# Optimization experiments

Measured on AMD Instinct MI355X. Metric: run time of the kernel, lower is better.

Reference implementation:

```python
import jax, jax.numpy as jnp
import numpy as np

EMB = 256
N_NODES = 100000
N_EDGES = 500000
N_REL = 10
REL_DIM = 64
HID = 128
HEADS = 4
HEAD_DIM = HID // HEADS


def setup_inputs() -> dict:
    key = jax.random.key(0)
    ks = jax.random.split(key, 16)
    s = lambda i, shape: jax.random.normal(ks[i], shape, dtype=jnp.float32) * 0.05
    return {
        "node_embeddings": jax.random.normal(ks[0], (N_NODES, EMB), dtype=jnp.float32),
        "edge_index": jax.random.randint(ks[1], (2, N_EDGES), 0, N_NODES),
        "relation_type": jax.random.randint(ks[2], (N_EDGES,), 0, N_REL),
        "rel_emb": s(3, (N_REL, REL_DIM)),
        "W_edge": s(4, (2 * EMB, HID)), "b_edge": jnp.zeros((HID,), jnp.float32),
        "W_q": s(5, (REL_DIM, HID)), "b_q": jnp.zeros((HID,), jnp.float32),
        "W_k": s(6, (HID, HID)), "b_k": jnp.zeros((HID,), jnp.float32),
        "W_v": s(7, (HID, HID)), "b_v": jnp.zeros((HID,), jnp.float32),
        "W_o1": s(8, (HID, HID)), "b_o1": jnp.zeros((HID,), jnp.float32),
        "W_o2": s(9, (HID, 1)), "b_o2": jnp.zeros((1,), jnp.float32),
    }


def reference(node_embeddings, edge_index, relation_type, rel_emb,
              W_edge, b_edge, W_q, b_q, W_k, b_k, W_v, b_v,
              W_o1, b_o1, W_o2, b_o2):
    # Gather endpoint features: [E, 2*EMB]
    src = node_embeddings[edge_index[0]]
    tgt = node_embeddings[edge_index[1]]
    edge_features = jnp.concatenate([src, tgt], axis=1)
    # Edge MLP (dropout is identity at eval): [E, HID]
    edge_hidden = jax.nn.relu(edge_features @ W_edge + b_edge)
    # Relation embedding lookup: [E, REL_DIM]
    rel = rel_emb[relation_type]
    E = edge_hidden.shape[0]
    Q = (rel @ W_q + b_q).reshape(E, HEADS, HEAD_DIM)
    K = (edge_hidden @ W_k + b_k).reshape(E, HEADS, HEAD_DIM)
    V = (edge_hidden @ W_v + b_v).reshape(E, HEADS, HEAD_DIM)
    scale = jnp.sqrt(jnp.float32(HEAD_DIM))
    scores = jnp.sum(Q * K, axis=-1) / scale          # [E, HEADS]
    attn = jax.nn.softmax(scores, axis=-1)            # softmax over heads
    attended = (attn[..., None] * V).reshape(E, HID)
    output = attended + edge_hidden
    # Output MLP: Linear->ReLU->Linear(1)
    h = jax.nn.relu(output @ W_o1 + b_o1)
    score = (h @ W_o2 + b_o2).squeeze(-1)             # [E]
    return score
```

## Files before the change

### kernel.cpp

```cpp
#include <hip/hip_runtime.h>

#define EMB   256
#define HID   128
#define RELD  64
#define NREL  10
#define TE    64

typedef __attribute__((ext_vector_type(8)))  short bf16x8;
typedef __attribute__((ext_vector_type(16))) float f32x16;

__device__ __forceinline__ float bf16_to_f32(unsigned short u) {
    union { unsigned int i; float f; } v;
    v.i = ((unsigned int)u) << 16;
    return v.f;
}

__device__ __forceinline__ unsigned short f32_to_bf16(float x) {
    union { unsigned int i; float f; } v;
    v.f = x;
    unsigned int b = v.i;
    unsigned int rounded = b + 0x7fffu + ((b >> 16) & 1u);
    return (unsigned short)(rounded >> 16);
}

template <bool F32>
__device__ __forceinline__ float ldx(const void* p, size_t i) {
    if (F32) return ((const float*)p)[i];
    return bf16_to_f32(((const unsigned short*)p)[i]);
}

__device__ __forceinline__ bool detect_f32(const void* nodeEmb) {
    const float* f = (const float*)nodeEmb;
    float x = f[(threadIdx.x & 63) * 997];
    bool sane = isfinite(x) && fabsf(x) < 1.0e6f;
    unsigned long long m = __ballot(sane);
    return __popcll(m) >= 48;
}

template <bool F32>
__device__ void prep_body(int vb, const void* W_edge, const void* W_k,
                          const void* W_v, const void* W_o1, const void* rel_emb,
                          const void* W_q, const void* b_q,
                          unsigned short* WTe, unsigned short* WTk,
                          unsigned short* WTv, unsigned short* WTo1, float* Qtab)
{
    if (vb < 448) {
        int idx = vb * 256 + threadIdx.x;
        if (idx < 65536) {
            int kc = idx >> 12, e = idx & 4095;
            int g = e >> 3, j = e & 7;
            int col = g & 127, kg = g >> 7;
            int k = kc * 32 + kg * 8 + j;
            WTe[idx] = f32_to_bf16(ldx<F32>(W_edge, (size_t)k * HID + col));
        } else if (idx < 65536 + 16384) {
            int i = idx - 65536;
            int kc = i >> 12, e = i & 4095;
            int g = e >> 3, j = e & 7;
            int col = g & 127, kg = (g >> 7) & 3;
            int k = kc * 32 + kg * 8 + j;
            WTk[i] = f32_to_bf16(ldx<F32>(W_k, (size_t)k * HID + col));
        } else if (idx < 65536 + 2 * 16384) {
            int i = idx - 65536 - 16384;
            int kc = i >> 12, e = i & 4095;
            int g = e >> 3, j = e & 7;
            int col = g & 127, kg = (g >> 7) & 3;
            int k = kc * 32 + kg * 8 + j;
            WTv[i] = f32_to_bf16(ldx<F32>(W_v, (size_t)k * HID + col));
        } else {
            int i = idx - 65536 - 2 * 16384;
            int kc = i >> 12, e = i & 4095;
            int g = e >> 3, j = e & 7;
            int col = g & 127, kg = (g >> 7) & 3;
            int k = kc * 32 + kg * 8 + j;
            WTo1[i] = f32_to_bf16(ldx<F32>(W_o1, (size_t)k * HID + col));
        }
    } else {
        const int t = threadIdx.x;
        const int c = t & (HID - 1);
        const int h = t >> 7;
        for (int r = h; r < NREL; r += 2) {
            float acc = 0.f;
            for (int d = 0; d < RELD; ++d)
                acc += ldx<F32>(rel_emb, r * RELD + d) * ldx<F32>(W_q, (size_t)d * HID + c);
            Qtab[r * HID + c] = acc + ldx<F32>(b_q, c);
        }
    }
}

__global__ void prep_kernel(const void* nodeEmb,
                            const void* W_edge, const void* W_k, const void* W_v,
                            const void* W_o1, const void* rel_emb, const void* W_q,
                            const void* b_q,
                            unsigned short* WTe, unsigned short* WTk,
                            unsigned short* WTv, unsigned short* WTo1, float* Qtab,
                            unsigned short* nodeBf16, int convBlocks,
                            unsigned long long nodeElems)
{
    bool f32 = detect_f32(nodeEmb);
    int b = blockIdx.x;
    if (b < convBlocks) {
        if (!f32) return;
        unsigned long long i = (unsigned long long)b * 2048ull + threadIdx.x * 8;
        if (i + 8 <= nodeElems) {
            const float* src = (const float*)nodeEmb + i;
            float4 f0 = *(const float4*)src;
            float4 f1 = *(const float4*)(src + 4);
            union { unsigned short us[8]; uint4 v; } pk;
            pk.us[0] = f32_to_bf16(f0.x); pk.us[1] = f32_to_bf16(f0.y);
            pk.us[2] = f32_to_bf16(f0.z); pk.us[3] = f32_to_bf16(f0.w);
            pk.us[4] = f32_to_bf16(f1.x); pk.us[5] = f32_to_bf16(f1.y);
            pk.us[6] = f32_to_bf16(f1.z); pk.us[7] = f32_to_bf16(f1.w);
            *(uint4*)(nodeBf16 + i) = pk.v;
        }
        return;
    }
    b -= convBlocks;
    if (f32) prep_body<true >(b, W_edge, W_k, W_v, W_o1, rel_emb, W_q, b_q,
                              WTe, WTk, WTv, WTo1, Qtab);
    else     prep_body<false>(b, W_edge, W_k, W_v, W_o1, rel_emb, W_q, b_q,
                              WTe, WTk, WTv, WTo1, Qtab);
}

struct __align__(16) Smem {
    unsigned short sHid[TE][136];
    union {
        unsigned short sA[TE][40];
        float sQf[NREL * HID];
    } u;
    unsigned short sB[4096];
    float sBias[5 * HID];
    float sSc[TE][4], sAttn[TE][4];
    float sPart[TE][2];
    int   sSrc[TE], sTgt[TE], sRel[TE];
};

__device__ __forceinline__ void gemm128(Smem& sm, const unsigned short* WT,
                                        f32x16* acc, int t, int rt, int cg2,
                                        int c, int h5)
{
    for (int kc = 0; kc < 4; ++kc) {
        const unsigned short* base = WT + kc * 4096;
        __syncthreads();
        *(uint4*)&sm.sB[(size_t)t * 8]         = *(const uint4*)(base + (size_t)t * 8);
        *(uint4*)&sm.sB[(size_t)(t + 256) * 8] = *(const uint4*)(base + (size_t)(t + 256) * 8);
        __syncthreads();
        #pragma unroll
        for (int s = 0; s < 2; ++s) {
            bf16x8 a = *(const bf16x8*)&sm.sHid[32 * rt + c][kc * 32 + s * 16 + h5 * 8];
            #pragma unroll
            for (int ct = 0; ct < 2; ++ct) {
                bf16x8 b = *(const bf16x8*)
                    &sm.sB[((s * 2 + h5) * 128 + 64 * cg2 + 32 * ct + c) * 8];
                acc[ct] = __builtin_amdgcn_mfma_f32_32x32x16_bf16(a, b, acc[ct], 0, 0, 0);
            }
        }
    }
}

template <bool F32, bool GBF16>
__device__ void fused_body(
    Smem& sm,
    const void* gsrc, const int* edgeIdx, const int* relType,
    const unsigned short* WTe, const unsigned short* WTk,
    const unsigned short* WTv, const unsigned short* WTo1,
    const void* b_edge, const void* b_k, const void* b_v,
    const void* b_o1, const void* W_o2, const void* b_o2,
    const float* Qtab, void* outp, int E)
{
    const int t   = threadIdx.x;
    const int l   = t & 63;
    const int w   = t >> 6;
    const int c   = l & 31;
    const int h5  = l >> 5;
    const int rt  = w & 1;
    const int cg2 = w >> 1;
    const int bs  = blockIdx.x * TE;

    if (t < TE) {
        int e = bs + t;
        if (e >= E) e = E - 1;
        if (e < 0)  e = 0;
        sm.sSrc[t] = edgeIdx[e];
        sm.sTgt[t] = edgeIdx[E + e];
        int r = relType[e];
        if (r < 0) r = 0;
        if (r >= NREL) r = NREL - 1;
        sm.sRel[t] = r;
    }
    for (int i = t; i < 5 * HID; i += 256) {
        int which = i >> 7, j = i & (HID - 1);
        float v = (which == 0) ? ldx<F32>(b_edge, j)
                : (which == 1) ? ldx<F32>(b_k, j)
                : (which == 2) ? ldx<F32>(b_v, j)
                : (which == 3) ? ldx<F32>(b_o1, j)
                               : ldx<F32>(W_o2, j);
        sm.sBias[i] = v;
    }
    __syncthreads();

    const int edge_s = t >> 2;
    const int grp    = t & 3;

    f32x16 acc[2];
    acc[0] = (f32x16)(0.0f); acc[1] = (f32x16)(0.0f);
    for (int kc = 0; kc < 16; ++kc) {
        __syncthreads();
        {
            int node = (kc < 8) ? sm.sSrc[edge_s] : sm.sTgt[edge_s];
            int col0 = (kc & 7) * 32 + grp * 8;
            if (GBF16) {
                *(uint4*)&sm.u.sA[edge_s][grp * 8] =
                    *(const uint4*)((const unsigned short*)gsrc +
                                    (size_t)node * EMB + col0);
            } else {
                const float* p = (const float*)gsrc + (size_t)node * EMB + col0;
                float4 f0 = *(const float4*)p;
                float4 f1 = *(const float4*)(p + 4);
                union { unsigned short us[8]; uint4 v; } pk;
                pk.us[0] = f32_to_bf16(f0.x); pk.us[1] = f32_to_bf16(f0.y);
                pk.us[2] = f32_to_bf16(f0.z); pk.us[3] = f32_to_bf16(f0.w);
                pk.us[4] = f32_to_bf16(f1.x); pk.us[5] = f32_to_bf16(f1.y);
                pk.us[6] = f32_to_bf16(f1.z); pk.us[7] = f32_to_bf16(f1.w);
                *(uint4*)&sm.u.sA[edge_s][grp * 8] = pk.v;
            }
        }
        {
            const unsigned short* base = WTe + kc * 4096;
            *(uint4*)&sm.sB[(size_t)t * 8]         = *(const uint4*)(base + (size_t)t * 8);
            *(uint4*)&sm.sB[(size_t)(t + 256) * 8] = *(const uint4*)(base + (size_t)(t + 256) * 8);
        }
        __syncthreads();
        #pragma unroll
        for (int s = 0; s < 2; ++s) {
            bf16x8 a = *(const bf16x8*)&sm.u.sA[32 * rt + c][s * 16 + h5 * 8];
            #pragma unroll
            for (int ct = 0; ct < 2; ++ct) {
                bf16x8 b = *(const bf16x8*)
                    &sm.sB[((s * 2 + h5) * 128 + 64 * cg2 + 32 * ct + c) * 8];
                acc[ct] = __builtin_amdgcn_mfma_f32_32x32x16_bf16(a, b, acc[ct], 0, 0, 0);
            }
        }
    }
    {
        #pragma unroll
        for (int ct = 0; ct < 2; ++ct) {
            int col = 64 * cg2 + 32 * ct + c;
            float bb = sm.sBias[col];
            #pragma unroll
            for (int r = 0; r < 16; ++r) {
                int erow = 32 * rt + (r & 3) + 8 * (r >> 2) + 4 * h5;
                sm.sHid[erow][col] = f32_to_bf16(fmaxf(acc[ct][r] + bb, 0.f));
            }
        }
    }
    __syncthreads();
    for (int i = t; i < NREL * HID; i += 256)
        sm.u.sQf[i] = Qtab[i];

    f32x16 kacc[2];
    kacc[0] = (f32x16)(0.0f); kacc[1] = (f32x16)(0.0f);
    gemm128(sm, WTk, kacc, t, rt, cg2, c, h5);

    {
        float ps[2][16];
        #pragma unroll
        for (int ct = 0; ct < 2; ++ct) {
            int col = 64 * cg2 + 32 * ct + c;
            float bk = sm.sBias[HID + col];
            #pragma unroll
            for (int r = 0; r < 16; ++r) {
                int erow = 32 * rt + (r & 3) + 8 * (r >> 2) + 4 * h5;
                ps[ct][r] = (kacc[ct][r] + bk) * sm.u.sQf[sm.sRel[erow] * HID + col];
            }
        }
        #pragma unroll
        for (int m = 1; m < 32; m <<= 1)
            #pragma unroll
            for (int ct = 0; ct < 2; ++ct)
                #pragma unroll
                for (int r = 0; r < 16; ++r)
                    ps[ct][r] += __shfl_xor(ps[ct][r], m, 64);
        if (c == 0) {
            const float inv = 0.17677669529663687f;
            #pragma unroll
            for (int ct = 0; ct < 2; ++ct) {
                int head = 2 * cg2 + ct;
                #pragma unroll
                for (int r = 0; r < 16; ++r) {
                    int erow = 32 * rt + (r & 3) + 8 * (r >> 2) + 4 * h5;
                    sm.sSc[erow][head] = ps[ct][r] * inv;
                }
            }
        }
    }
    __syncthreads();
    if (t < TE) {
        float s0 = sm.sSc[t][0], s1 = sm.sSc[t][1];
        float s2 = sm.sSc[t][2], s3 = sm.sSc[t][3];
        float m = fmaxf(fmaxf(s0, s1), fmaxf(s2, s3));
        float e0 = expf(s0 - m), e1 = expf(s1 - m);
        float e2 = expf(s2 - m), e3 = expf(s3 - m);
        float den = e0 + e1 + e2 + e3;
        sm.sAttn[t][0] = e0 / den; sm.sAttn[t][1] = e1 / den;
        sm.sAttn[t][2] = e2 / den; sm.sAttn[t][3] = e3 / den;
    }
    __syncthreads();

    f32x16 vacc[2];
    vacc[0] = (f32x16)(0.0f); vacc[1] = (f32x16)(0.0f);
    gemm128(sm, WTv, vacc, t, rt, cg2, c, h5);
    {
        #pragma unroll
        for (int ct = 0; ct < 2; ++ct) {
            int col  = 64 * cg2 + 32 * ct + c;
            int head = 2 * cg2 + ct;
            float bv = sm.sBias[2 * HID + col];
            #pragma unroll
            for (int r = 0; r < 16; ++r) {
                int erow = 32 * rt + (r & 3) + 8 * (r >> 2) + 4 * h5;
                float at = sm.sAttn[erow][head];
                float hv = bf16_to_f32(sm.sHid[erow][col]);
                sm.sHid[erow][col] = f32_to_bf16(at * (vacc[ct][r] + bv) + hv);
            }
        }
    }

    f32x16 oacc[2];
    oacc[0] = (f32x16)(0.0f); oacc[1] = (f32x16)(0.0f);
    gemm128(sm, WTo1, oacc, t, rt, cg2, c, h5);
    {
        float pr[16];
        #pragma unroll
        for (int r = 0; r < 16; ++r) pr[r] = 0.f;
        #pragma unroll
        for (int ct = 0; ct < 2; ++ct) {
            int col = 64 * cg2 + 32 * ct + c;
            float bo = sm.sBias[3 * HID + col];
            float wo = sm.sBias[4 * HID + col];
            #pragma unroll
            for (int r = 0; r < 16; ++r)
                pr[r] += fmaxf(oacc[ct][r] + bo, 0.f) * wo;
        }
        #pragma unroll
        for (int m = 1; m < 32; m <<= 1)
            #pragma unroll
            for (int r = 0; r < 16; ++r)
                pr[r] += __shfl_xor(pr[r], m, 64);
        if (c == 0) {
            #pragma unroll
            for (int r = 0; r < 16; ++r) {
                int erow = 32 * rt + (r & 3) + 8 * (r >> 2) + 4 * h5;
                sm.sPart[erow][cg2] = pr[r];
            }
        }
    }
    __syncthreads();
    if (t < TE) {
        int ge = bs + t;
        if (ge < E) {
            float val = sm.sPart[t][0] + sm.sPart[t][1] + ldx<F32>(b_o2, 0);
            if (F32) ((float*)outp)[ge] = val;
            else     ((unsigned short*)outp)[ge] = f32_to_bf16(val);
        }
    }
}

__global__ __launch_bounds__(256, 4) void RelationAttentionMLPHead_10539849744626_kernel(
    const void* nodeEmb, const unsigned short* nodeBf16, int useConv,
    const int* edgeIdx, const int* relType,
    const unsigned short* WTe, const unsigned short* WTk,
    const unsigned short* WTv, const unsigned short* WTo1,
    const void* b_edge, const void* b_k, const void* b_v,
    const void* b_o1, const void* W_o2, const void* b_o2,
    const float* Qtab, void* outp, int E)
{
    __shared__ Smem sm;
    if (detect_f32(nodeEmb)) {
        if (useConv)
            fused_body<true, true >(sm, nodeBf16, edgeIdx, relType, WTe, WTk, WTv, WTo1,
                                    b_edge, b_k, b_v, b_o1, W_o2, b_o2, Qtab, outp, E);
        else
            fused_body<true, false>(sm, nodeEmb, edgeIdx, relType, WTe, WTk, WTv, WTo1,
                                    b_edge, b_k, b_v, b_o1, W_o2, b_o2, Qtab, outp, E);
    } else {
        fused_body<false, true>(sm, nodeEmb, edgeIdx, relType, WTe, WTk, WTv, WTo1,
                                b_edge, b_k, b_v, b_o1, W_o2, b_o2, Qtab, outp, E);
    }
}

extern "C" void kernel_launch(void* const* d_in, const int* in_sizes, int n_in,
                              void* d_out, int out_size, void* d_ws, size_t ws_size,
                              hipStream_t stream) {
    (void)n_in;

    const void* nodeEmb = d_in[0];
    const int*  edgeIdx = (const int*)d_in[1];
    const int*  relType = (const int*)d_in[2];
    const void* rel_emb = d_in[3];
    const void* W_edge  = d_in[4];
    const void* b_edge  = d_in[5];
    const void* W_q     = d_in[6];
    const void* b_q     = d_in[7];
    const void* W_k     = d_in[8];
    const void* b_k     = d_in[9];
    const void* W_v     = d_in[10];
    const void* b_v     = d_in[11];
    const void* W_o1    = d_in[12];
    const void* b_o1    = d_in[13];
    const void* W_o2    = d_in[14];
    const void* b_o2    = d_in[15];

    int E = out_size;
    if (E <= 0) E = in_sizes ? in_sizes[2] : 0;
    if (E <= 0) E = 500000;

    unsigned long long nodeElems =
        (in_sizes && in_sizes[0] > 0) ? (unsigned long long)in_sizes[0] : 25600000ull;

    char* ws = (char*)d_ws;
    float*          Qtab     = (float*)ws;
    unsigned short* WTe      = (unsigned short*)(ws + 8192);
    unsigned short* WTk      = (unsigned short*)(ws + 139264);
    unsigned short* WTv      = (unsigned short*)(ws + 172032);
    unsigned short* WTo1     = (unsigned short*)(ws + 204800);
    unsigned short* nodeBf16 = (unsigned short*)(ws + 237568);

    size_t need = 237568ull + nodeElems * 2ull;
    int useConv = (ws_size >= need) ? 1 : 0;
    int convBlocks = useConv ? (int)((nodeElems + 2047ull) / 2048ull) : 0;

    prep_kernel<<<convBlocks + 449, 256, 0, stream>>>(
        nodeEmb, W_edge, W_k, W_v, W_o1, rel_emb, W_q, b_q,
        WTe, WTk, WTv, WTo1, Qtab, nodeBf16, convBlocks, nodeElems);

    int grid = (E + TE - 1) / TE;
    if (grid < 1) grid = 1;

    RelationAttentionMLPHead_10539849744626_kernel<<<grid, 256, 0, stream>>>(
        nodeEmb, nodeBf16, useConv, edgeIdx, relType, WTe, WTk, WTv, WTo1,
        b_edge, b_k, b_v, b_o1, W_o2, b_o2, Qtab, d_out, E);
}
```

Measured before the change: 447.3 us.

## Load GEMM operands directly from global memory and fuse K/V projections

Drops the shared-memory staging of the gathered node rows and weight tiles. Each lane now loads its MFMA A and B fragments straight from global memory, which removes the two barriers per k-chunk. The K and V GEMMs are merged into a single loop that shares the A fragment, and the Q table load moves into the prologue. The cost is more register pressure and uncoalesced, repeated global and L2 reads of the weights and node rows, since each wave fetches its own fragments.

```diff
diff --git a/kernel.cpp b/kernel.cpp
--- a/kernel.cpp
+++ b/kernel.cpp
@@ -123,37 +123,27 @@
 
 struct __align__(16) Smem {
     unsigned short sHid[TE][136];
-    union {
-        unsigned short sA[TE][40];
-        float sQf[NREL * HID];
-    } u;
-    unsigned short sB[4096];
+    float sQf[NREL * HID];
     float sBias[5 * HID];
     float sSc[TE][4], sAttn[TE][4];
     float sPart[TE][2];
     int   sSrc[TE], sTgt[TE], sRel[TE];
 };
 
-__device__ __forceinline__ void gemm128(Smem& sm, const unsigned short* WT,
-                                        f32x16* acc, int t, int rt, int cg2,
-                                        int c, int h5)
-{
-    for (int kc = 0; kc < 4; ++kc) {
-        const unsigned short* base = WT + kc * 4096;
-        __syncthreads();
-        *(uint4*)&sm.sB[(size_t)t * 8]         = *(const uint4*)(base + (size_t)t * 8);
-        *(uint4*)&sm.sB[(size_t)(t + 256) * 8] = *(const uint4*)(base + (size_t)(t + 256) * 8);
-        __syncthreads();
-        #pragma unroll
-        for (int s = 0; s < 2; ++s) {
-            bf16x8 a = *(const bf16x8*)&sm.sHid[32 * rt + c][kc * 32 + s * 16 + h5 * 8];
-            #pragma unroll
-            for (int ct = 0; ct < 2; ++ct) {
-                bf16x8 b = *(const bf16x8*)
-                    &sm.sB[((s * 2 + h5) * 128 + 64 * cg2 + 32 * ct + c) * 8];
-                acc[ct] = __builtin_amdgcn_mfma_f32_32x32x16_bf16(a, b, acc[ct], 0, 0, 0);
-            }
-        }
+template <bool GBF16>
+__device__ __forceinline__ bf16x8 loadA8(const void* row, int off) {
+    if (GBF16) {
+        return *(const bf16x8*)((const unsigned short*)row + off);
+    } else {
+        const float* p = (const float*)row + off;
+        float4 f0 = *(const float4*)p;
+        float4 f1 = *(const float4*)(p + 4);
+        union { unsigned short us[8]; bf16x8 v; } pk;
+        pk.us[0] = f32_to_bf16(f0.x); pk.us[1] = f32_to_bf16(f0.y);
+        pk.us[2] = f32_to_bf16(f0.z); pk.us[3] = f32_to_bf16(f0.w);
+        pk.us[4] = f32_to_bf16(f1.x); pk.us[5] = f32_to_bf16(f1.y);
+        pk.us[6] = f32_to_bf16(f1.z); pk.us[7] = f32_to_bf16(f1.w);
+        return pk.v;
     }
 }
 
@@ -175,6 +165,7 @@
     const int rt  = w & 1;
     const int cg2 = w >> 1;
     const int bs  = blockIdx.x * TE;
+    const int mye = 32 * rt + c;
 
     if (t < TE) {
         int e = bs + t;
@@ -196,47 +187,34 @@
                                : ldx<F32>(W_o2, j);
         sm.sBias[i] = v;
     }
-    __syncthreads();
-
-    const int edge_s = t >> 2;
-    const int grp    = t & 3;
+    for (int i = t; i < NREL * HID; i += 256)
+        sm.sQf[i] = Qtab[i];
+    __syncthreads();
+
+    const void* rowSrc;
+    const void* rowTgt;
+    if (GBF16) {
+        rowSrc = (const void*)((const unsigned short*)gsrc + (size_t)sm.sSrc[mye] * EMB);
+        rowTgt = (const void*)((const unsigned short*)gsrc + (size_t)sm.sTgt[mye] * EMB);
+    } else {
+        rowSrc = (const void*)((const float*)gsrc + (size_t)sm.sSrc[mye] * EMB);
+        rowTgt = (const void*)((const float*)gsrc + (size_t)sm.sTgt[mye] * EMB);
+    }
+
+    const int bu = (h5 * 128 + 64 * cg2 + c) * 8;
 
     f32x16 acc[2];
     acc[0] = (f32x16)(0.0f); acc[1] = (f32x16)(0.0f);
+    #pragma unroll
     for (int kc = 0; kc < 16; ++kc) {
-        __syncthreads();
-        {
-            int node = (kc < 8) ? sm.sSrc[edge_s] : sm.sTgt[edge_s];
-            int col0 = (kc & 7) * 32 + grp * 8;
-            if (GBF16) {
-                *(uint4*)&sm.u.sA[edge_s][grp * 8] =
-                    *(const uint4*)((const unsigned short*)gsrc +
-                                    (size_t)node * EMB + col0);
-            } else {
-                const float* p = (const float*)gsrc + (size_t)node * EMB + col0;
-                float4 f0 = *(const float4*)p;
-                float4 f1 = *(const float4*)(p + 4);
-                union { unsigned short us[8]; uint4 v; } pk;
-                pk.us[0] = f32_to_bf16(f0.x); pk.us[1] = f32_to_bf16(f0.y);
-                pk.us[2] = f32_to_bf16(f0.z); pk.us[3] = f32_to_bf16(f0.w);
-                pk.us[4] = f32_to_bf16(f1.x); pk.us[5] = f32_to_bf16(f1.y);
-                pk.us[6] = f32_to_bf16(f1.z); pk.us[7] = f32_to_bf16(f1.w);
-                *(uint4*)&sm.u.sA[edge_s][grp * 8] = pk.v;
-            }
-        }
-        {
-            const unsigned short* base = WTe + kc * 4096;
-            *(uint4*)&sm.sB[(size_t)t * 8]         = *(const uint4*)(base + (size_t)t * 8);
-            *(uint4*)&sm.sB[(size_t)(t + 256) * 8] = *(const uint4*)(base + (size_t)(t + 256) * 8);
-        }
-        __syncthreads();
+        const void* row = (kc < 8) ? rowSrc : rowTgt;
+        const int cb = (kc & 7) * 32;
         #pragma unroll
         for (int s = 0; s < 2; ++s) {
-            bf16x8 a = *(const bf16x8*)&sm.u.sA[32 * rt + c][s * 16 + h5 * 8];
+            bf16x8 a = loadA8<GBF16>(row, cb + s * 16 + h5 * 8);
             #pragma unroll
             for (int ct = 0; ct < 2; ++ct) {
-                bf16x8 b = *(const bf16x8*)
-                    &sm.sB[((s * 2 + h5) * 128 + 64 * cg2 + 32 * ct + c) * 8];
+                bf16x8 b = *(const bf16x8*)(WTe + kc * 4096 + s * 2048 + ct * 256 + bu);
                 acc[ct] = __builtin_amdgcn_mfma_f32_32x32x16_bf16(a, b, acc[ct], 0, 0, 0);
             }
         }
@@ -254,12 +232,24 @@
         }
     }
     __syncthreads();
-    for (int i = t; i < NREL * HID; i += 256)
-        sm.u.sQf[i] = Qtab[i];
-
-    f32x16 kacc[2];
+
+    f32x16 kacc[2], vacc[2];
     kacc[0] = (f32x16)(0.0f); kacc[1] = (f32x16)(0.0f);
-    gemm128(sm, WTk, kacc, t, rt, cg2, c, h5);
+    vacc[0] = (f32x16)(0.0f); vacc[1] = (f32x16)(0.0f);
+    #pragma unroll
+    for (int kc = 0; kc < 4; ++kc) {
+        #pragma unroll
+        for (int s = 0; s < 2; ++s) {
+            bf16x8 a = *(const bf16x8*)&sm.sHid[mye][kc * 32 + s * 16 + h5 * 8];
+            #pragma unroll
+            for (int ct = 0; ct < 2; ++ct) {
+                bf16x8 bk = *(const bf16x8*)(WTk + kc * 4096 + s * 2048 + ct * 256 + bu);
+                bf16x8 bv = *(const bf16x8*)(WTv + kc * 4096 + s * 2048 + ct * 256 + bu);
+                kacc[ct] = __builtin_amdgcn_mfma_f32_32x32x16_bf16(a, bk, kacc[ct], 0, 0, 0);
+                vacc[ct] = __builtin_amdgcn_mfma_f32_32x32x16_bf16(a, bv, vacc[ct], 0, 0, 0);
+            }
+        }
+    }
 
     {
         float ps[2][16];
@@ -270,7 +260,7 @@
             #pragma unroll
             for (int r = 0; r < 16; ++r) {
                 int erow = 32 * rt + (r & 3) + 8 * (r >> 2) + 4 * h5;
-                ps[ct][r] = (kacc[ct][r] + bk) * sm.u.sQf[sm.sRel[erow] * HID + col];
+                ps[ct][r] = (kacc[ct][r] + bk) * sm.sQf[sm.sRel[erow] * HID + col];
             }
         }
         #pragma unroll
@@ -306,9 +296,6 @@
     }
     __syncthreads();
 
-    f32x16 vacc[2];
-    vacc[0] = (f32x16)(0.0f); vacc[1] = (f32x16)(0.0f);
-    gemm128(sm, WTv, vacc, t, rt, cg2, c, h5);
     {
         #pragma unroll
         for (int ct = 0; ct < 2; ++ct) {
@@ -324,10 +311,22 @@
             }
         }
     }
+    __syncthreads();
 
     f32x16 oacc[2];
     oacc[0] = (f32x16)(0.0f); oacc[1] = (f32x16)(0.0f);
-    gemm128(sm, WTo1, oacc, t, rt, cg2, c, h5);
+    #pragma unroll
+    for (int kc = 0; kc < 4; ++kc) {
+        #pragma unroll
+        for (int s = 0; s < 2; ++s) {
+            bf16x8 a = *(const bf16x8*)&sm.sHid[mye][kc * 32 + s * 16 + h5 * 8];
+            #pragma unroll
+            for (int ct = 0; ct < 2; ++ct) {
+                bf16x8 b = *(const bf16x8*)(WTo1 + kc * 4096 + s * 2048 + ct * 256 + bu);
+                oacc[ct] = __builtin_amdgcn_mfma_f32_32x32x16_bf16(a, b, oacc[ct], 0, 0, 0);
+            }
+        }
+    }
     {
         float pr[16];
         #pragma unroll
```

Measured after the change: 452.9 us. About the same (+1.3%).

## Double-buffer LDS staging with direct global-to-LDS loads and 128-edge tiles

Applied to the files above, without the earlier changes.

Doubles the edge tile to 128 edges per 512-thread block. It replaces the single-buffered A/B staging with double-buffered LDS tiles filled by global_load_lds, so the next K-chunk's gather and weight loads overlap the current MFMAs. The hidden tile is re-laid out in k-major 8-element groups to match the new load pattern, and Qtab is loaded once up front instead of sharing a union. This aims to hide gather latency and halve the weight re-staging per edge, at the cost of more LDS per block and possibly lower occupancy.

```diff
diff --git a/kernel.cpp b/kernel.cpp
--- a/kernel.cpp
+++ b/kernel.cpp
@@ -4,7 +4,7 @@
 #define HID   128
 #define RELD  64
 #define NREL  10
-#define TE    64
+#define TE    128
 
 typedef __attribute__((ext_vector_type(8)))  short bf16x8;
 typedef __attribute__((ext_vector_type(16))) float f32x16;
@@ -35,6 +35,12 @@
     bool sane = isfinite(x) && fabsf(x) < 1.0e6f;
     unsigned long long m = __ballot(sane);
     return __popcll(m) >= 48;
+}
+
+__device__ __forceinline__ void gload16(const void* g, void* l) {
+    __builtin_amdgcn_global_load_lds(
+        (const __attribute__((address_space(1))) unsigned int*)g,
+        (__attribute__((address_space(3))) unsigned int*)l, 16, 0, 0);
 }
 
 template <bool F32>
@@ -122,39 +128,19 @@
 }
 
 struct __align__(16) Smem {
-    unsigned short sHid[TE][136];
-    union {
-        unsigned short sA[TE][40];
-        float sQf[NREL * HID];
-    } u;
-    unsigned short sB[4096];
+    unsigned short sHid[16 * 128 * 8];
+    unsigned short SA[2][4096];
+    unsigned short SB[2][4096];
+    float sQf[NREL * HID];
     float sBias[5 * HID];
-    float sSc[TE][4], sAttn[TE][4];
+    float sSc[TE][4];
+    float sAttn[TE][4];
     float sPart[TE][2];
     int   sSrc[TE], sTgt[TE], sRel[TE];
 };
 
-__device__ __forceinline__ void gemm128(Smem& sm, const unsigned short* WT,
-                                        f32x16* acc, int t, int rt, int cg2,
-                                        int c, int h5)
-{
-    for (int kc = 0; kc < 4; ++kc) {
-        const unsigned short* base = WT + kc * 4096;
-        __syncthreads();
-        *(uint4*)&sm.sB[(size_t)t * 8]         = *(const uint4*)(base + (size_t)t * 8);
-        *(uint4*)&sm.sB[(size_t)(t + 256) * 8] = *(const uint4*)(base + (size_t)(t + 256) * 8);
-        __syncthreads();
-        #pragma unroll
-        for (int s = 0; s < 2; ++s) {
-            bf16x8 a = *(const bf16x8*)&sm.sHid[32 * rt + c][kc * 32 + s * 16 + h5 * 8];
-            #pragma unroll
-            for (int ct = 0; ct < 2; ++ct) {
-                bf16x8 b = *(const bf16x8*)
-                    &sm.sB[((s * 2 + h5) * 128 + 64 * cg2 + 32 * ct + c) * 8];
-                acc[ct] = __builtin_amdgcn_mfma_f32_32x32x16_bf16(a, b, acc[ct], 0, 0, 0);
-            }
-        }
-    }
+__device__ __forceinline__ int shid_idx(int row, int k) {
+    return (((k >> 3) * 128 + row) << 3) + (k & 7);
 }
 
 template <bool F32, bool GBF16>
@@ -172,9 +158,10 @@
     const int w   = t >> 6;
     const int c   = l & 31;
     const int h5  = l >> 5;
-    const int rt  = w & 1;
-    const int cg2 = w >> 1;
+    const int rt  = w >> 1;
+    const int cg2 = w & 1;
     const int bs  = blockIdx.x * TE;
+    const int aRow = 32 * rt + c;
 
     if (t < TE) {
         int e = bs + t;
@@ -187,7 +174,7 @@
         if (r >= NREL) r = NREL - 1;
         sm.sRel[t] = r;
     }
-    for (int i = t; i < 5 * HID; i += 256) {
+    for (int i = t; i < 5 * HID; i += 512) {
         int which = i >> 7, j = i & (HID - 1);
         float v = (which == 0) ? ldx<F32>(b_edge, j)
                 : (which == 1) ? ldx<F32>(b_k, j)
@@ -196,50 +183,88 @@
                                : ldx<F32>(W_o2, j);
         sm.sBias[i] = v;
     }
-    __syncthreads();
-
-    const int edge_s = t >> 2;
-    const int grp    = t & 3;
+    for (int i = t; i < NREL * HID; i += 512)
+        sm.sQf[i] = Qtab[i];
+    __syncthreads();
+
+    const int    stS   = t >> 8;
+    const int    stH5  = (t >> 7) & 1;
+    const int    stRow = t & 127;
+    const size_t rowOffS = (size_t)sm.sSrc[stRow] * EMB;
+    const size_t rowOffT = (size_t)sm.sTgt[stRow] * EMB;
+    const int    colSub  = stS * 16 + stH5 * 8;
+    char* const  ldsWaveA0 = (char*)sm.SA[0] + w * 1024;
+    char* const  ldsWaveA1 = (char*)sm.SA[1] + w * 1024;
+    char* const  ldsWaveB0 = (char*)sm.SB[0] + w * 1024;
+    char* const  ldsWaveB1 = (char*)sm.SB[1] + w * 1024;
+
+    #define STAGE_A(kc, buf)                                                     \
+    {                                                                            \
+        size_t eoff = (((kc) < 8) ? rowOffS : rowOffT)                           \
+                      + (size_t)(((kc) & 7) * 32 + colSub);                      \
+        if (GBF16) {                                                             \
+            gload16((const unsigned short*)gsrc + eoff,                          \
+                    (buf) ? ldsWaveA1 : ldsWaveA0);                              \
+        } else {                                                                 \
+            const float* p_ = (const float*)gsrc + eoff;                         \
+            float4 f0_ = *(const float4*)p_;                                     \
+            float4 f1_ = *(const float4*)(p_ + 4);                               \
+            union { unsigned short us[8]; uint4 v; } pk_;                        \
+            pk_.us[0] = f32_to_bf16(f0_.x); pk_.us[1] = f32_to_bf16(f0_.y);      \
+            pk_.us[2] = f32_to_bf16(f0_.z); pk_.us[3] = f32_to_bf16(f0_.w);      \
+            pk_.us[4] = f32_to_bf16(f1_.x); pk_.us[5] = f32_to_bf16(f1_.y);      \
+            pk_.us[6] = f32_to_bf16(f1_.z); pk_.us[7] = f32_to_bf16(f1_.w);      \
+            *(uint4*)((char*)sm.SA[(buf)] + t * 16) = pk_.v;                     \
+        }                                                                        \
+    }
+
+    #define STAGE_B(WT, kc, buf)                                                 \
+        gload16((WT) + (kc) * 4096 + t * 8, (buf) ? ldsWaveB1 : ldsWaveB0);
+
+    #define MFMA_SA(buf, accv)                                                   \
+    {                                                                            \
+        const char* sa_ = (const char*)sm.SA[(buf)];                             \
+        const char* sb_ = (const char*)sm.SB[(buf)];                             \
+        _Pragma("unroll")                                                        \
+        for (int s_ = 0; s_ < 2; ++s_) {                                         \
+            bf16x8 a_ = *(const bf16x8*)(sa_ + ((s_ * 256 + h5 * 128 + aRow) << 4)); \
+            _Pragma("unroll")                                                    \
+            for (int ct_ = 0; ct_ < 2; ++ct_) {                                  \
+                bf16x8 b_ = *(const bf16x8*)                                     \
+                    (sb_ + ((s_ * 256 + h5 * 128 + 64 * cg2 + 32 * ct_ + c) << 4)); \
+                accv[ct_] = __builtin_amdgcn_mfma_f32_32x32x16_bf16(             \
+                                a_, b_, accv[ct_], 0, 0, 0);                     \
+            }                                                                    \
+        }                                                                        \
+    }
+
+    #define MFMA_H(kc, buf, accv)                                                \
+    {                                                                            \
+        const char* sb_ = (const char*)sm.SB[(buf)];                             \
+        _Pragma("unroll")                                                        \
+        for (int s_ = 0; s_ < 2; ++s_) {                                         \
+            bf16x8 a_ = *(const bf16x8*)((const char*)sm.sHid +                  \
+                         ((((kc) * 4 + s_ * 2 + h5) * 128 + aRow) << 4));        \
+            _Pragma("unroll")                                                    \
+            for (int ct_ = 0; ct_ < 2; ++ct_) {                                  \
+                bf16x8 b_ = *(const bf16x8*)                                     \
+                    (sb_ + ((s_ * 256 + h5 * 128 + 64 * cg2 + 32 * ct_ + c) << 4)); \
+                accv[ct_] = __builtin_amdgcn_mfma_f32_32x32x16_bf16(             \
+                                a_, b_, accv[ct_], 0, 0, 0);                     \
+            }                                                                    \
+        }                                                                        \
+    }
 
     f32x16 acc[2];
     acc[0] = (f32x16)(0.0f); acc[1] = (f32x16)(0.0f);
+    STAGE_A(0, 0); STAGE_B(WTe, 0, 0);
+    __syncthreads();
+    #pragma unroll
     for (int kc = 0; kc < 16; ++kc) {
+        int buf = kc & 1;
+        if (kc < 15) { STAGE_A(kc + 1, buf ^ 1); STAGE_B(WTe, kc + 1, buf ^ 1); }
+        MFMA_SA(buf, acc);
         __syncthreads();
-        {
-            int node = (kc < 8) ? sm.sSrc[edge_s] : sm.sTgt[edge_s];
-            int col0 = (kc & 7) * 32 + grp * 8;
-            if (GBF16) {
-                *(uint4*)&sm.u.sA[edge_s][grp * 8] =
-                    *(const uint4*)((const unsigned short*)gsrc +
-                                    (size_t)node * EMB + col0);
-            } else {
-                const float* p = (const float*)gsrc + (size_t)node * EMB + col0;
-                float4 f0 = *(const float4*)p;
-                float4 f1 = *(const float4*)(p + 4);
-                union { unsigned short us[8]; uint4 v; } pk;
-                pk.us[0] = f32_to_bf16(f0.x); pk.us[1] = f32_to_bf16(f0.y);
-                pk.us[2] = f32_to_bf16(f0.z); pk.us[3] = f32_to_bf16(f0.w);
-                pk.us[4] = f32_to_bf16(f1.x); pk.us[5] = f32_to_bf16(f1.y);
-                pk.us[6] = f32_to_bf16(f1.z); pk.us[7] = f32_to_bf16(f1.w);
-                *(uint4*)&sm.u.sA[edge_s][grp * 8] = pk.v;
-            }
-        }
-        {
-            const unsigned short* base = WTe + kc * 4096;
-            *(uint4*)&sm.sB[(size_t)t * 8]         = *(const uint4*)(base + (size_t)t * 8);
-            *(uint4*)&sm.sB[(size_t)(t + 256) * 8] = *(const uint4*)(base + (size_t)(t + 256) * 8);
-        }
-        __syncthreads();
-        #pragma unroll
-        for (int s = 0; s < 2; ++s) {
-            bf16x8 a = *(const bf16x8*)&sm.u.sA[32 * rt + c][s * 16 + h5 * 8];
-            #pragma unroll
-            for (int ct = 0; ct < 2; ++ct) {
-                bf16x8 b = *(const bf16x8*)
-                    &sm.sB[((s * 2 + h5) * 128 + 64 * cg2 + 32 * ct + c) * 8];
-                acc[ct] = __builtin_amdgcn_mfma_f32_32x32x16_bf16(a, b, acc[ct], 0, 0, 0);
-            }
-        }
     }
     {
         #pragma unroll
@@ -249,17 +274,22 @@
             #pragma unroll
             for (int r = 0; r < 16; ++r) {
                 int erow = 32 * rt + (r & 3) + 8 * (r >> 2) + 4 * h5;
-                sm.sHid[erow][col] = f32_to_bf16(fmaxf(acc[ct][r] + bb, 0.f));
+                sm.sHid[shid_idx(erow, col)] = f32_to_bf16(fmaxf(acc[ct][r] + bb, 0.f));
             }
         }
     }
-    __syncthreads();
-    for (int i = t; i < NREL * HID; i += 256)
-        sm.u.sQf[i] = Qtab[i];
 
     f32x16 kacc[2];
     kacc[0] = (f32x16)(0.0f); kacc[1] = (f32x16)(0.0f);
-    gemm128(sm, WTk, kacc, t, rt, cg2, c, h5);
+    STAGE_B(WTk, 0, 0);
+    __syncthreads();
+    #pragma unroll
+    for (int kc = 0; kc < 4; ++kc) {
+        int buf = kc & 1;
+        if (kc < 3) STAGE_B(WTk, kc + 1, buf ^ 1);
+        MFMA_H(kc, buf, kacc);
+        __syncthreads();
+    }
 
     {
         float ps[2][16];
@@ -270,7 +300,7 @@
             #pragma unroll
             for (int r = 0; r < 16; ++r) {
                 int erow = 32 * rt + (r & 3) + 8 * (r >> 2) + 4 * h5;
-                ps[ct][r] = (kacc[ct][r] + bk) * sm.u.sQf[sm.sRel[erow] * HID + col];
+                ps[ct][r] = (kacc[ct][r] + bk) * sm.sQf[sm.sRel[erow] * HID + col];
             }
         }
         #pragma unroll
@@ -308,7 +338,16 @@
 
     f32x16 vacc[2];
     vacc[0] = (f32x16)(0.0f); vacc[1] = (f32x16)(0.0f);
-    gemm128(sm, WTv, vacc, t, rt, cg2, c, h5);
+    STAGE_B(WTv, 0, 0);
+    __syncthreads();
+    #pragma unroll
+    for (int kc = 0; kc < 4; ++kc) {
+        int buf = kc & 1;
+        if (kc < 3) STAGE_B(WTv, kc + 1, buf ^ 1);
+        MFMA_H(kc, buf, vacc);
+        __syncthreads();
+    }
+
     {
         #pragma unroll
         for (int ct = 0; ct < 2; ++ct) {
@@ -319,15 +358,25 @@
             for (int r = 0; r < 16; ++r) {
                 int erow = 32 * rt + (r & 3) + 8 * (r >> 2) + 4 * h5;
                 float at = sm.sAttn[erow][head];
-                float hv = bf16_to_f32(sm.sHid[erow][col]);
-                sm.sHid[erow][col] = f32_to_bf16(at * (vacc[ct][r] + bv) + hv);
+                int   si = shid_idx(erow, col);
+                float hv = bf16_to_f32(sm.sHid[si]);
+                sm.sHid[si] = f32_to_bf16(at * (vacc[ct][r] + bv) + hv);
             }
         }
     }
+    __syncthreads();
 
     f32x16 oacc[2];
     oacc[0] = (f32x16)(0.0f); oacc[1] = (f32x16)(0.0f);
-    gemm128(sm, WTo1, oacc, t, rt, cg2, c, h5);
+    STAGE_B(WTo1, 0, 0);
+    __syncthreads();
+    #pragma unroll
+    for (int kc = 0; kc < 4; ++kc) {
+        int buf = kc & 1;
+        if (kc < 3) STAGE_B(WTo1, kc + 1, buf ^ 1);
+        MFMA_H(kc, buf, oacc);
+        __syncthreads();
+    }
     {
         float pr[16];
         #pragma unroll
@@ -363,9 +412,14 @@
             else     ((unsigned short*)outp)[ge] = f32_to_bf16(val);
         }
     }
-}
-
-__global__ __launch_bounds__(256, 4) void RelationAttentionMLPHead_10539849744626_kernel(
+
+    #undef STAGE_A
+    #undef STAGE_B
+    #undef MFMA_SA
+    #undef MFMA_H
+}
+
+__global__ __launch_bounds__(512, 4) void RelationAttentionMLPHead_10539849744626_kernel(
     const void* nodeEmb, const unsigned short* nodeBf16, int useConv,
     const int* edgeIdx, const int* relType,
     const unsigned short* WTe, const unsigned short* WTk,
@@ -436,7 +490,7 @@
     int grid = (E + TE - 1) / TE;
     if (grid < 1) grid = 1;
 
-    RelationAttentionMLPHead_10539849744626_kernel<<<grid, 256, 0, stream>>>(
+    RelationAttentionMLPHead_10539849744626_kernel<<<grid, 512, 0, stream>>>(
         nodeEmb, nodeBf16, useConv, edgeIdx, relType, WTe, WTk, WTv, WTo1,
         b_edge, b_k, b_v, b_o1, W_o2, b_o2, Qtab, d_out, E);
 }
```

Result: slower. 459.5 us (+2.7%).
